# Performance work log

Measured on AMD Instinct MI355X. Metric: run time of the kernel, lower is better.

The kernel has to match this reference:

```python
import jax, jax.numpy as jnp
import numpy as np

QUERY_DIM = 512
KEY_DIM = 512
HIDDEN_DIM = 512


def setup_inputs() -> dict:
    key = jax.random.key(0)
    k1, k2, k3, k4, k5 = jax.random.split(key, 5)
    B, S = 32, 2048
    query = jax.random.normal(k1, (B, QUERY_DIM), dtype=jnp.float32)
    keys = jax.random.normal(k2, (B, S, KEY_DIM), dtype=jnp.float32)
    # nn.Linear weights stored as [out_features, in_features]
    Wq = jax.random.normal(k3, (HIDDEN_DIM, QUERY_DIM), dtype=jnp.float32) / np.sqrt(QUERY_DIM)
    Wk = jax.random.normal(k4, (HIDDEN_DIM, KEY_DIM), dtype=jnp.float32) / np.sqrt(KEY_DIM)
    w_att = jax.random.normal(k5, (HIDDEN_DIM,), dtype=jnp.float32) / np.sqrt(HIDDEN_DIM)
    return {"query": query, "keys": keys, "Wq": Wq, "Wk": Wk, "w_att": w_att}


def reference(query, keys, Wq, Wk, w_att):
    # values defaults to keys
    values = keys
    q = query @ Wq.T                               # [B, H]
    k = jnp.einsum('bsd,hd->bsh', keys, Wk)        # [B, S, H]
    combined = jnp.tanh(q[:, None, :] + k)         # [B, S, H]
    scores = jnp.einsum('bsh,h->bs', combined, w_att)  # [B, S]
    attn = jax.nn.softmax(scores, axis=-1)         # [B, S]
    out = jnp.einsum('bs,bsd->bd', attn, values)   # [B, D]
    return (out, attn)
```

## Files before the change

kernel.cpp:

```cpp
#include <hip/hip_runtime.h>
#include <hip/hip_fp16.h>

typedef _Float16 f16x8 __attribute__((ext_vector_type(8)));
typedef _Float16 f16x4 __attribute__((ext_vector_type(4)));
typedef float f32x4 __attribute__((ext_vector_type(4)));

#define WS_QV 0
#define WS_BF 65536
#define WS_SP 589824
#define WS_VP 1114112

__global__ __launch_bounds__(256) void prep_kernel(
    const float* __restrict__ query, const float* __restrict__ Wq,
    const float* __restrict__ Wk, float* __restrict__ qv,
    _Float16* __restrict__ bfrag) {
  const int blk = blockIdx.x, tid = threadIdx.x;
  if (blk < 64) {
    const int b = blk >> 1;
    const int h = ((blk & 1) << 8) + tid;
    const float4* qr = (const float4*)(query + (size_t)b * 512);
    const float4* wr = (const float4*)(Wq + (size_t)h * 512);
    float acc = 0.f;
#pragma unroll 8
    for (int i = 0; i < 128; ++i) {
      float4 a = qr[i], w = wr[i];
      acc += a.x * w.x + a.y * w.y + a.z * w.z + a.w * w.w;
    }
    qv[b * 512 + h] = acc;
  } else {
    const int u = (blk - 64) * 4 + (tid >> 6);
    const int l = tid & 63;
    const int col = ((u >> 4) << 4) + (l & 15);
    const int k0 = ((u & 15) << 5) + ((l >> 4) << 3);
    const float4* src = (const float4*)(Wk + (size_t)col * 512 + k0);
    float4 x = src[0], y = src[1];
    f16x8 v;
    v[0] = (_Float16)x.x; v[1] = (_Float16)x.y;
    v[2] = (_Float16)x.z; v[3] = (_Float16)x.w;
    v[4] = (_Float16)y.x; v[5] = (_Float16)y.y;
    v[6] = (_Float16)y.z; v[7] = (_Float16)y.w;
    *(f16x8*)(bfrag + (size_t)u * 512 + l * 8) = v;
  }
}

__global__ __launch_bounds__(512, 4) void gemm_kernel(
    const float* __restrict__ keys, const _Float16* __restrict__ bfrag,
    const float* __restrict__ qv, const float* __restrict__ w_att,
    float* __restrict__ spart_out) {
  __shared__ __align__(128) unsigned char lds[16384];
  __shared__ float sred[256];
  const int tid = threadIdx.x, w = tid >> 6, l = tid & 63;
  const int bid = ((blockIdx.x & 7) << 8) + (blockIdx.x >> 3);
  const int rt = bid >> 1, hs = bid & 1;
  const int row0 = rt * 64;
  const int b = row0 >> 11;
  const int wm = w >> 2, wn = w & 3;

  const int sr = tid >> 3, sc8 = (tid & 7) << 3;
  const float* gsrc = keys + (size_t)(row0 + sr) * 512 + sc8;
  const int wbyte = sr * 128 + (sc8 << 1);
  const int wswz = (sr & 7) << 4;

  float4 stg[2];
  stg[0] = ((const float4*)gsrc)[0];
  stg[1] = ((const float4*)gsrc)[1];
  {
    f16x8 h;
    h[0] = (_Float16)stg[0].x; h[1] = (_Float16)stg[0].y;
    h[2] = (_Float16)stg[0].z; h[3] = (_Float16)stg[0].w;
    h[4] = (_Float16)stg[1].x; h[5] = (_Float16)stg[1].y;
    h[6] = (_Float16)stg[1].z; h[7] = (_Float16)stg[1].w;
    *(f16x8*)(lds + (wbyte ^ wswz)) = h;
  }
  __syncthreads();

  f32x4 acc[2][4];
#pragma unroll
  for (int mt = 0; mt < 2; ++mt)
#pragma unroll
    for (int nt = 0; nt < 4; ++nt) {
      acc[mt][nt][0] = 0.f; acc[mt][nt][1] = 0.f;
      acc[mt][nt][2] = 0.f; acc[mt][nt][3] = 0.f;
    }

  const int aswz = (l & 7) << 4;
  const int akslot = (l >> 4) << 4;
  const int arow = (wm * 32 + (l & 15)) * 128;

#pragma unroll
  for (int c = 0; c < 8; ++c) {
    if (c < 7) {
      const float4* g = (const float4*)(gsrc + (c + 1) * 64);
      stg[0] = g[0]; stg[1] = g[1];
    }
    __builtin_amdgcn_sched_barrier(0);

    const unsigned char* buf = lds + (c & 1) * 8192;
#pragma unroll
    for (int ks = 0; ks < 2; ++ks) {
      const int KS = c * 2 + ks;
      f16x8 af[2];
#pragma unroll
      for (int mt = 0; mt < 2; ++mt)
        af[mt] = *(const f16x8*)(buf + arow + mt * 2048 +
                                 ((ks * 64 + akslot) ^ aswz));
#pragma unroll
      for (int ng = 0; ng < 2; ++ng) {
        f16x8 bf[2];
#pragma unroll
        for (int n2 = 0; n2 < 2; ++n2) {
          const int u = ((hs << 4) + (wn << 2) + ng * 2 + n2) * 16 + KS;
          bf[n2] = *(const f16x8*)(bfrag + (size_t)u * 512 + l * 8);
        }
#pragma unroll
        for (int mt = 0; mt < 2; ++mt)
#pragma unroll
          for (int n2 = 0; n2 < 2; ++n2)
            acc[mt][ng * 2 + n2] = __builtin_amdgcn_mfma_f32_16x16x32_f16(
                af[mt], bf[n2], acc[mt][ng * 2 + n2], 0, 0, 0);
      }
    }
    __builtin_amdgcn_sched_barrier(0);

    if (c < 7) {
      unsigned char* db = lds + ((c + 1) & 1) * 8192;
      f16x8 h;
      h[0] = (_Float16)stg[0].x; h[1] = (_Float16)stg[0].y;
      h[2] = (_Float16)stg[0].z; h[3] = (_Float16)stg[0].w;
      h[4] = (_Float16)stg[1].x; h[5] = (_Float16)stg[1].y;
      h[6] = (_Float16)stg[1].z; h[7] = (_Float16)stg[1].w;
      *(f16x8*)(db + (wbyte ^ wswz)) = h;
    }
    __syncthreads();
  }

  float rs[8];
#pragma unroll
  for (int i = 0; i < 8; ++i) rs[i] = 0.f;
#pragma unroll
  for (int nt = 0; nt < 4; ++nt) {
    const int h = (hs << 8) + (wn << 6) + (nt << 4) + (l & 15);
    const float q = qv[b * 512 + h];
    const float wa = w_att[h];
#pragma unroll
    for (int mt = 0; mt < 2; ++mt)
#pragma unroll
      for (int r = 0; r < 4; ++r) {
        float x = q + acc[mt][nt][r];
        float e = __expf(x + x);
        float t = 1.f - __fdividef(2.f, e + 1.f);
        rs[mt * 4 + r] = __builtin_fmaf(t, wa, rs[mt * 4 + r]);
      }
  }
#pragma unroll
  for (int st = 1; st <= 8; st <<= 1)
#pragma unroll
    for (int i = 0; i < 8; ++i)
      rs[i] += __shfl_xor(rs[i], st, 64);

  {
    const int idx = l & 15;
    if (idx < 8) {
      float v = rs[0];
#pragma unroll
      for (int i = 1; i < 8; ++i) v = (idx == i) ? rs[i] : v;
      const int rloc = ((idx >> 2) << 4) + ((l >> 4) << 2) + (idx & 3);
      sred[w * 32 + rloc] = v;
    }
  }
  __syncthreads();
  if (tid < 64) {
    const int wmq = tid >> 5, rl = tid & 31;
    float s = sred[(wmq * 4 + 0) * 32 + rl] + sred[(wmq * 4 + 1) * 32 + rl] +
              sred[(wmq * 4 + 2) * 32 + rl] + sred[(wmq * 4 + 3) * 32 + rl];
    spart_out[hs * 65536 + row0 + tid] = s;
  }
}

__global__ __launch_bounds__(256) void softv_kernel(
    const float* __restrict__ keys, const float* __restrict__ spart,
    float* __restrict__ attn, _Float16* __restrict__ vpart) {
  __shared__ float pe[2048];
  __shared__ float red_mx[4], red_se[4];
  __shared__ float4 comb[128];
  const int tid = threadIdx.x;
  const int b = blockIdx.x >> 5, sc = blockIdx.x & 31;
  const float* p0 = spart + (size_t)b * 2048;
  const float* p1 = spart + 65536 + (size_t)b * 2048;

  float sv[8];
  float mx = -1e30f;
#pragma unroll
  for (int i = 0; i < 8; ++i) {
    sv[i] = p0[i * 256 + tid] + p1[i * 256 + tid];
    mx = fmaxf(mx, sv[i]);
  }
#pragma unroll
  for (int st = 32; st >= 1; st >>= 1) mx = fmaxf(mx, __shfl_xor(mx, st, 64));
  if ((tid & 63) == 0) red_mx[tid >> 6] = mx;
  __syncthreads();
  mx = fmaxf(fmaxf(red_mx[0], red_mx[1]), fmaxf(red_mx[2], red_mx[3]));

  float se = 0.f;
#pragma unroll
  for (int i = 0; i < 8; ++i) {
    float e = __expf(sv[i] - mx);
    pe[i * 256 + tid] = e;
    se += e;
  }
#pragma unroll
  for (int st = 32; st >= 1; st >>= 1) se += __shfl_xor(se, st, 64);
  if ((tid & 63) == 0) red_se[tid >> 6] = se;
  __syncthreads();
  se = red_se[0] + red_se[1] + red_se[2] + red_se[3];
  const float rinv = 1.f / se;

  if (tid < 64) {
    int s = sc * 64 + tid;
    attn[(size_t)b * 2048 + s] = pe[s] * rinv;
  }

  const int c4 = tid & 127, rg = tid >> 7;
  const float4* kb = (const float4*)(keys + ((size_t)(b * 2048 + sc * 64 + rg * 32)) * 512);
  float4 a; a.x = 0.f; a.y = 0.f; a.z = 0.f; a.w = 0.f;
#pragma unroll 4
  for (int i = 0; i < 32; ++i) {
    float p = pe[sc * 64 + rg * 32 + i];
    float4 kv = kb[(size_t)i * 128 + c4];
    a.x = __builtin_fmaf(p, kv.x, a.x);
    a.y = __builtin_fmaf(p, kv.y, a.y);
    a.z = __builtin_fmaf(p, kv.z, a.z);
    a.w = __builtin_fmaf(p, kv.w, a.w);
  }
  if (rg) comb[c4] = a;
  __syncthreads();
  if (!rg) {
    float4 o = comb[c4];
    f16x4 h;
    h[0] = (_Float16)((a.x + o.x) * rinv);
    h[1] = (_Float16)((a.y + o.y) * rinv);
    h[2] = (_Float16)((a.z + o.z) * rinv);
    h[3] = (_Float16)((a.w + o.w) * rinv);
    *(f16x4*)(vpart + (size_t)blockIdx.x * 512 + c4 * 4) = h;
  }
}

__global__ __launch_bounds__(256) void reduce_kernel(
    const _Float16* __restrict__ vpart, float* __restrict__ out) {
  const int t = blockIdx.x * 256 + threadIdx.x;
  const int b = t >> 9, d = t & 511;
  float s = 0.f;
#pragma unroll
  for (int sc = 0; sc < 32; ++sc)
    s += (float)vpart[((size_t)(b * 32 + sc)) * 512 + d];
  out[t] = s;
}

extern "C" void kernel_launch(void* const* d_in, const int* in_sizes, int n_in,
                              void* d_out, int out_size, void* d_ws, size_t ws_size,
                              hipStream_t stream) {
  const float* query = (const float*)d_in[0];
  const float* keys  = (const float*)d_in[1];
  const float* Wq    = (const float*)d_in[2];
  const float* Wk    = (const float*)d_in[3];
  const float* w_att = (const float*)d_in[4];
  float* out  = (float*)d_out;
  float* attn = out + 16384;
  char* ws = (char*)d_ws;
  float*    qv     = (float*)(ws + WS_QV);
  _Float16* bfrag  = (_Float16*)(ws + WS_BF);
  float*    spart  = (float*)(ws + WS_SP);
  _Float16* vpart  = (_Float16*)(ws + WS_VP);

  prep_kernel<<<192, 256, 0, stream>>>(query, Wq, Wk, qv, bfrag);
  gemm_kernel<<<2048, 512, 0, stream>>>(keys, bfrag, qv, w_att, spart);
  softv_kernel<<<1024, 256, 0, stream>>>(keys, spart, attn, vpart);
  reduce_kernel<<<64, 256, 0, stream>>>(vpart, out);
}
```

Before: 113.6 us.

## Load fp32 keys directly into LDS and compute full hidden dim per block

```diff
diff --git a/kernel.cpp b/kernel.cpp
--- a/kernel.cpp
+++ b/kernel.cpp
@@ -7,8 +7,13 @@
 
 #define WS_QV 0
 #define WS_BF 65536
-#define WS_SP 589824
-#define WS_VP 1114112
+#define WS_SC 589824
+#define WS_VP 851968
+
+#define GLOAD_LDS16(g, l)                                              \
+  __builtin_amdgcn_global_load_lds(                                    \
+      (const __attribute__((address_space(1))) void*)(g),              \
+      (__attribute__((address_space(3))) void*)(l), 16, 0, 0)
 
 __global__ __launch_bounds__(256) void prep_kernel(
     const float* __restrict__ query, const float* __restrict__ Wq,
@@ -43,93 +48,79 @@
   }
 }
 
-__global__ __launch_bounds__(512, 4) void gemm_kernel(
+__global__ __launch_bounds__(512) void gemm_kernel(
     const float* __restrict__ keys, const _Float16* __restrict__ bfrag,
     const float* __restrict__ qv, const float* __restrict__ w_att,
-    float* __restrict__ spart_out) {
-  __shared__ __align__(128) unsigned char lds[16384];
+    float* __restrict__ scores) {
+  __shared__ __align__(128) unsigned char lds[32768];
   __shared__ float sred[256];
   const int tid = threadIdx.x, w = tid >> 6, l = tid & 63;
-  const int bid = ((blockIdx.x & 7) << 8) + (blockIdx.x >> 3);
-  const int rt = bid >> 1, hs = bid & 1;
-  const int row0 = rt * 64;
+  const int row0 = blockIdx.x * 64;
   const int b = row0 >> 11;
   const int wm = w >> 2, wn = w & 3;
 
-  const int sr = tid >> 3, sc8 = (tid & 7) << 3;
-  const float* gsrc = keys + (size_t)(row0 + sr) * 512 + sc8;
-  const int wbyte = sr * 128 + (sc8 << 1);
-  const int wswz = (sr & 7) << 4;
-
-  float4 stg[2];
-  stg[0] = ((const float4*)gsrc)[0];
-  stg[1] = ((const float4*)gsrc)[1];
-  {
-    f16x8 h;
-    h[0] = (_Float16)stg[0].x; h[1] = (_Float16)stg[0].y;
-    h[2] = (_Float16)stg[0].z; h[3] = (_Float16)stg[0].w;
-    h[4] = (_Float16)stg[1].x; h[5] = (_Float16)stg[1].y;
-    h[6] = (_Float16)stg[1].z; h[7] = (_Float16)stg[1].w;
-    *(f16x8*)(lds + (wbyte ^ wswz)) = h;
-  }
-  __syncthreads();
-
-  f32x4 acc[2][4];
+  const int r0s = 8 * w + (l >> 4);
+  const char* gb = (const char*)keys;
+  const int soff0 = ((l & 15) * 16) ^ (((r0s + 0) & 7) << 4);
+  const int soff1 = ((l & 15) * 16) ^ (((r0s + 4) & 7) << 4);
+  const size_t grow0 = (size_t)(row0 + r0s) * 2048;
+  const size_t grow1 = (size_t)(row0 + r0s + 4) * 2048;
+
+  GLOAD_LDS16(gb + grow0 + 0 * 256 + soff0, lds + (2 * w + 0) * 1024);
+  GLOAD_LDS16(gb + grow1 + 0 * 256 + soff1, lds + (2 * w + 1) * 1024);
+  __syncthreads();
+
+  f32x4 acc[2][8];
 #pragma unroll
   for (int mt = 0; mt < 2; ++mt)
 #pragma unroll
-    for (int nt = 0; nt < 4; ++nt) {
+    for (int nt = 0; nt < 8; ++nt) {
       acc[mt][nt][0] = 0.f; acc[mt][nt][1] = 0.f;
       acc[mt][nt][2] = 0.f; acc[mt][nt][3] = 0.f;
     }
 
-  const int aswz = (l & 7) << 4;
-  const int akslot = (l >> 4) << 4;
-  const int arow = (wm * 32 + (l & 15)) * 128;
-
-#pragma unroll
-  for (int c = 0; c < 8; ++c) {
-    if (c < 7) {
-      const float4* g = (const float4*)(gsrc + (c + 1) * 64);
-      stg[0] = g[0]; stg[1] = g[1];
-    }
-    __builtin_amdgcn_sched_barrier(0);
-
-    const unsigned char* buf = lds + (c & 1) * 8192;
+  const int arow = wm * 32 + (l & 15);
+  const int akb = (l >> 4) << 5;
+
+#pragma unroll
+  for (int kt = 0; kt < 8; ++kt) {
+    if (kt < 7) {
+      const size_t kadd = (size_t)(kt + 1) * 256;
+      unsigned char* db = lds + ((kt + 1) & 1) * 16384;
+      GLOAD_LDS16(gb + grow0 + kadd + soff0, db + (2 * w + 0) * 1024);
+      GLOAD_LDS16(gb + grow1 + kadd + soff1, db + (2 * w + 1) * 1024);
+    }
+
+    const unsigned char* buf = lds + (kt & 1) * 16384;
 #pragma unroll
     for (int ks = 0; ks < 2; ++ks) {
-      const int KS = c * 2 + ks;
+      const int KST = kt * 2 + ks;
       f16x8 af[2];
 #pragma unroll
+      for (int mt = 0; mt < 2; ++mt) {
+        const int rr = arow + mt * 16;
+        const int cb = (ks * 128 + akb) ^ ((rr & 7) << 4);
+        const float4 x = *(const float4*)(buf + rr * 256 + cb);
+        const float4 y = *(const float4*)(buf + rr * 256 + (cb ^ 16));
+        f16x8 h;
+        h[0] = (_Float16)x.x; h[1] = (_Float16)x.y;
+        h[2] = (_Float16)x.z; h[3] = (_Float16)x.w;
+        h[4] = (_Float16)y.x; h[5] = (_Float16)y.y;
+        h[6] = (_Float16)y.z; h[7] = (_Float16)y.w;
+        af[mt] = h;
+      }
+      f16x8 bf[8];
+#pragma unroll
+      for (int nt = 0; nt < 8; ++nt) {
+        const int u = (wn * 8 + nt) * 16 + KST;
+        bf[nt] = *(const f16x8*)(bfrag + (size_t)u * 512 + l * 8);
+      }
+#pragma unroll
       for (int mt = 0; mt < 2; ++mt)
-        af[mt] = *(const f16x8*)(buf + arow + mt * 2048 +
-                                 ((ks * 64 + akslot) ^ aswz));
-#pragma unroll
-      for (int ng = 0; ng < 2; ++ng) {
-        f16x8 bf[2];
-#pragma unroll
-        for (int n2 = 0; n2 < 2; ++n2) {
-          const int u = ((hs << 4) + (wn << 2) + ng * 2 + n2) * 16 + KS;
-          bf[n2] = *(const f16x8*)(bfrag + (size_t)u * 512 + l * 8);
-        }
-#pragma unroll
-        for (int mt = 0; mt < 2; ++mt)
-#pragma unroll
-          for (int n2 = 0; n2 < 2; ++n2)
-            acc[mt][ng * 2 + n2] = __builtin_amdgcn_mfma_f32_16x16x32_f16(
-                af[mt], bf[n2], acc[mt][ng * 2 + n2], 0, 0, 0);
-      }
-    }
-    __builtin_amdgcn_sched_barrier(0);
-
-    if (c < 7) {
-      unsigned char* db = lds + ((c + 1) & 1) * 8192;
-      f16x8 h;
-      h[0] = (_Float16)stg[0].x; h[1] = (_Float16)stg[0].y;
-      h[2] = (_Float16)stg[0].z; h[3] = (_Float16)stg[0].w;
-      h[4] = (_Float16)stg[1].x; h[5] = (_Float16)stg[1].y;
-      h[6] = (_Float16)stg[1].z; h[7] = (_Float16)stg[1].w;
-      *(f16x8*)(db + (wbyte ^ wswz)) = h;
+#pragma unroll
+        for (int nt = 0; nt < 8; ++nt)
+          acc[mt][nt] = __builtin_amdgcn_mfma_f32_16x16x32_f16(
+              af[mt], bf[nt], acc[mt][nt], 0, 0, 0);
     }
     __syncthreads();
   }
@@ -138,8 +129,8 @@
 #pragma unroll
   for (int i = 0; i < 8; ++i) rs[i] = 0.f;
 #pragma unroll
-  for (int nt = 0; nt < 4; ++nt) {
-    const int h = (hs << 8) + (wn << 6) + (nt << 4) + (l & 15);
+  for (int nt = 0; nt < 8; ++nt) {
+    const int h = (wn << 7) + (nt << 4) + (l & 15);
     const float q = qv[b * 512 + h];
     const float wa = w_att[h];
 #pragma unroll
@@ -173,26 +164,25 @@
     const int wmq = tid >> 5, rl = tid & 31;
     float s = sred[(wmq * 4 + 0) * 32 + rl] + sred[(wmq * 4 + 1) * 32 + rl] +
               sred[(wmq * 4 + 2) * 32 + rl] + sred[(wmq * 4 + 3) * 32 + rl];
-    spart_out[hs * 65536 + row0 + tid] = s;
+    scores[row0 + tid] = s;
   }
 }
 
 __global__ __launch_bounds__(256) void softv_kernel(
-    const float* __restrict__ keys, const float* __restrict__ spart,
+    const float* __restrict__ keys, const float* __restrict__ scores,
     float* __restrict__ attn, _Float16* __restrict__ vpart) {
   __shared__ float pe[2048];
   __shared__ float red_mx[4], red_se[4];
   __shared__ float4 comb[128];
   const int tid = threadIdx.x;
   const int b = blockIdx.x >> 5, sc = blockIdx.x & 31;
-  const float* p0 = spart + (size_t)b * 2048;
-  const float* p1 = spart + 65536 + (size_t)b * 2048;
+  const float* srow = scores + (size_t)b * 2048;
 
   float sv[8];
   float mx = -1e30f;
 #pragma unroll
   for (int i = 0; i < 8; ++i) {
-    sv[i] = p0[i * 256 + tid] + p1[i * 256 + tid];
+    sv[i] = srow[i * 256 + tid];
     mx = fmaxf(mx, sv[i]);
   }
 #pragma unroll
@@ -269,11 +259,11 @@
   char* ws = (char*)d_ws;
   float*    qv     = (float*)(ws + WS_QV);
   _Float16* bfrag  = (_Float16*)(ws + WS_BF);
-  float*    spart  = (float*)(ws + WS_SP);
+  float*    scores = (float*)(ws + WS_SC);
   _Float16* vpart  = (_Float16*)(ws + WS_VP);
 
   prep_kernel<<<192, 256, 0, stream>>>(query, Wq, Wk, qv, bfrag);
-  gemm_kernel<<<2048, 512, 0, stream>>>(keys, bfrag, qv, w_att, spart);
-  softv_kernel<<<1024, 256, 0, stream>>>(keys, spart, attn, vpart);
+  gemm_kernel<<<1024, 512, 0, stream>>>(keys, bfrag, qv, w_att, scores);
+  softv_kernel<<<1024, 256, 0, stream>>>(keys, scores, attn, vpart);
   reduce_kernel<<<64, 256, 0, stream>>>(vpart, out);
 }
```

After: 116.9 us. 2.9% more time.
